# Performance work log

Measured on AMD Instinct MI355X. Metric: run time of the kernel, lower is better.

Reference implementation:

```python
import jax, jax.numpy as jnp
import numpy as np

V = 1024      # token vocab
C = 8         # n_codebooks
T = 256       # seg_len
BP = 4        # block_pairs (n_latent_blocks)
K = 512       # latent_vocab_size (codebook entries)
E = 128       # emb_dim
D = 128       # latent_dim / d_model
BETA = 0.05
NB = 6 * BP   # decoder sequence length = 24
NH = 4
HD = D // NH
FF = 512
R = 8
IN_FLAT = NB * D
OUT = T * C * V
B = 32


def setup_inputs() -> dict:
    key = jax.random.key(0)
    ks = jax.random.split(key, 20)
    n = lambda i, shape, s=0.02: jax.random.normal(ks[i], shape, jnp.float32) * s
    return {
        "tokens_prev": jax.random.randint(ks[0], (B, T, C), 0, V, jnp.int32),
        "tokens_curr": jax.random.randint(ks[1], (B, T, C), 0, V, jnp.int32),
        "tokens_next": jax.random.randint(ks[2], (B, T, C), 0, V, jnp.int32),
        "emb": n(3, (V, E)),
        "conv1_w": n(4, (4 * D, E * C, 3)),
        "conv1_b": jnp.zeros((4 * D,), jnp.float32),
        "conv2_w": n(5, (2 * D, 4 * D, 1)),
        "conv2_b": jnp.zeros((2 * D,), jnp.float32),
        "cb_instru": jax.random.uniform(ks[6], (K, D), jnp.float32, -1.0 / K, 1.0 / K),
        "cb_vocal": jax.random.uniform(ks[7], (K, D), jnp.float32, -1.0 / K, 1.0 / K),
        "pos": n(8, (1, NB, D), 1.0),
        "attn_in_w": n(9, (3 * D, D)),
        "attn_in_b": jnp.zeros((3 * D,), jnp.float32),
        "attn_out_w": n(10, (D, D)),
        "attn_out_b": jnp.zeros((D,), jnp.float32),
        "ln1_g": jnp.ones((D,), jnp.float32),
        "ln1_b": jnp.zeros((D,), jnp.float32),
        "lin1_w": n(11, (FF, D)),
        "lin1_b": jnp.zeros((FF,), jnp.float32),
        "lin2_w": n(12, (D, FF)),
        "lin2_b": jnp.zeros((D,), jnp.float32),
        "ln2_g": jnp.ones((D,), jnp.float32),
        "ln2_b": jnp.zeros((D,), jnp.float32),
        "lora_a": n(13, (R, IN_FLAT), 0.01),
        "lora_b": n(14, (OUT, R), 0.01),
    }


def _conv1d(x, w, b, pad):
    # x: (B, Cin, L), w: (Cout, Cin, Kw)
    y = jax.lax.conv_general_dilated(x, w, window_strides=(1,), padding=[(pad, pad)],
                                     dimension_numbers=("NCH", "OIH", "NCH"))
    return y + b[None, :, None]


def _encode(tokens, emb, w1, b1, w2, b2):
    Bb, Tt, Cc = tokens.shape
    x = emb[tokens].reshape(Bb, Tt, -1).transpose(0, 2, 1)       # (B, C*E, T)
    x = jax.nn.relu(_conv1d(x, w1, b1, 1))                        # (B, 4D, T)
    x = jax.nn.relu(_conv1d(x, w2, b2, 0))                        # (B, 2D, T)
    # AdaptiveAvgPool1d(BP) with T % BP == 0 -> mean over contiguous chunks
    x = x.reshape(Bb, 2 * D, BP, Tt // BP).mean(-1).transpose(0, 2, 1)  # (B, BP, 2D)
    return x[..., :D], x[..., D:]


def _vq(z, codebook):
    # z: (B, N, D); eval-mode VQ (no EMA update)
    Bb, N, Dd = z.shape
    flat = z.reshape(-1, Dd)
    dist = (jnp.sum(flat * flat, axis=1, keepdims=True)
            - 2.0 * flat @ codebook.T
            + jnp.sum(codebook * codebook, axis=1))
    codes = jnp.argmin(dist, axis=1)
    z_q = codebook[codes].reshape(Bb, N, Dd)
    commit = jnp.mean((z - jax.lax.stop_gradient(z_q)) ** 2)
    loss = BETA * commit
    z_q_st = z + jax.lax.stop_gradient(z_q - z)
    return z_q_st, codes.reshape(Bb, N), loss


def _layer_norm(x, g, b):
    mu = x.mean(-1, keepdims=True)
    var = ((x - mu) ** 2).mean(-1, keepdims=True)
    return (x - mu) * jax.lax.rsqrt(var + 1e-5) * g + b


def _tf_layer(x, in_w, in_b, out_w, out_b, g1, b1, w1, bb1, w2, bb2, g2, b2):
    # Post-norm TransformerEncoderLayer (relu, eval/no-dropout). x: (B, S, D)
    Bb, S, Dd = x.shape
    qkv = x @ in_w.T + in_b
    q, k, v = jnp.split(qkv, 3, axis=-1)
    q = q.reshape(Bb, S, NH, HD).transpose(0, 2, 1, 3)
    k = k.reshape(Bb, S, NH, HD).transpose(0, 2, 1, 3)
    v = v.reshape(Bb, S, NH, HD).transpose(0, 2, 1, 3)
    attn = jax.nn.softmax(jnp.einsum("bhsd,bhtd->bhst", q, k) / np.sqrt(HD), axis=-1)
    o = jnp.einsum("bhst,bhtd->bhsd", attn, v).transpose(0, 2, 1, 3).reshape(Bb, S, Dd)
    x = _layer_norm(x + o @ out_w.T + out_b, g1, b1)
    ff = jax.nn.relu(x @ w1.T + bb1) @ w2.T + bb2
    return _layer_norm(x + ff, g2, b2)


def reference(tokens_prev, tokens_curr, tokens_next, emb, conv1_w, conv1_b,
              conv2_w, conv2_b, cb_instru, cb_vocal, pos, attn_in_w, attn_in_b,
              attn_out_w, attn_out_b, ln1_g, ln1_b, lin1_w, lin1_b, lin2_w,
              lin2_b, ln2_g, ln2_b, lora_a, lora_b):
    p_i, p_v = _encode(tokens_prev, emb, conv1_w, conv1_b, conv2_w, conv2_b)
    c_i, c_v = _encode(tokens_curr, emb, conv1_w, conv1_b, conv2_w, conv2_b)
    n_i, n_v = _encode(tokens_next, emb, conv1_w, conv1_b, conv2_w, conv2_b)
    p_i_q, _, l1 = _vq(p_i, cb_instru)
    c_i_q, _, l2 = _vq(c_i, cb_instru)
    n_i_q, _, l3 = _vq(n_i, cb_instru)
    p_v_q, _, l4 = _vq(p_v, cb_vocal)
    c_v_q, _, l5 = _vq(c_v, cb_vocal)
    n_v_q, _, l6 = _vq(n_v, cb_vocal)
    vq_loss = l1 + l2 + l3 + l4 + l5 + l6
    z = jnp.concatenate([p_i_q, p_v_q, c_i_q, c_v_q, n_i_q, n_v_q], axis=1)  # (B, 24, D)
    z = z + pos[:, :z.shape[1], :]
    z = _tf_layer(z, attn_in_w, attn_in_b, attn_out_w, attn_out_b,
                  ln1_g, ln1_b, lin1_w, lin1_b, lin2_w, lin2_b, ln2_g, ln2_b)
    Bb = z.shape[0]
    flat = z.reshape(Bb, -1)
    logits = (flat @ lora_a.T) @ lora_b.T          # (B, T*C*V)
    logits = logits.reshape(Bb, T, C, V)
    logp = jax.nn.log_softmax(logits, axis=-1)
    nll = -jnp.take_along_axis(logp, tokens_curr[..., None].astype(jnp.int32), axis=-1)
    recon_loss = nll.mean()
    total_loss = recon_loss + vq_loss
    return total_loss
```

## Files before the change

### kernel.cpp

```cpp
#include <hip/hip_runtime.h>
#include <hip/hip_bf16.h>
#include <cstdint>
#include <cstddef>

typedef __attribute__((ext_vector_type(8))) short short8;
typedef __attribute__((ext_vector_type(4))) float floatx4;


__device__ __forceinline__ ushort f2bf(float f) {
    union { float f; unsigned int u; } x; x.f = f;
    unsigned int r = (x.u + 0x7fffu + ((x.u >> 16) & 1u)) >> 16;
    return (ushort)r;
}
__device__ __forceinline__ float bf2f(ushort u) {
    union { unsigned int u; float f; } x; x.u = ((unsigned int)u) << 16;
    return x.f;
}

__global__ __launch_bounds__(256) void prep_all(
    const float* __restrict__ emb, const float* __restrict__ w1,
    const float* __restrict__ w2, const float* __restrict__ cbi,
    const float* __restrict__ cbv, const float* __restrict__ aiw,
    const float* __restrict__ aow, const float* __restrict__ l1w,
    const float* __restrict__ l2w,
    ushort* __restrict__ ebf, ushort* __restrict__ w1bf, ushort* __restrict__ w2bf,
    float* __restrict__ cbiT, float* __restrict__ cbvT,
    ushort* __restrict__ aiwbf, ushort* __restrict__ aowbf,
    ushort* __restrict__ l1wbf, ushort* __restrict__ l2wbf,
    float* __restrict__ accum)
{
    int idx = blockIdx.x * 256 + threadIdx.x;
    if (idx < 4) accum[idx] = 0.f;
    if (idx < 131072) {
        ebf[idx] = f2bf(emb[idx]);
    } else if (idx < 262144) {
        int j = idx - 131072; w2bf[j] = f2bf(w2[j]);
    } else if (idx < 327680) {
        int j = idx - 262144; cbiT[(j & 127) * 512 + (j >> 7)] = cbi[j];
    } else if (idx < 393216) {
        int j = idx - 327680; cbvT[(j & 127) * 512 + (j >> 7)] = cbv[j];
    } else if (idx < 442368) {
        int j = idx - 393216; aiwbf[j] = f2bf(aiw[j]);
    } else if (idx < 475136) {
        int j = idx - 442368; aowbf[j] = f2bf(aow[j]);
    } else if (idx < 540672) {
        int j = idx - 475136; l1wbf[j] = f2bf(l1w[j]);
    } else if (idx < 606208) {
        int j = idx - 540672; l2wbf[j] = f2bf(l2w[j]);
    } else if (idx < 2179072) {
        int j = idx - 606208;
        int e  = j & 127;
        int co = (j >> 7) & 511;
        int cc = (j >> 16) & 7;
        int kw = j >> 19;
        w1bf[j] = f2bf(w1[(co * 1024 + cc * 128 + e) * 3 + kw]);
    }
}

__global__ __launch_bounds__(512, 4) void conv1_mfma(
    const int* __restrict__ tp, const int* __restrict__ tcu, const int* __restrict__ tn,
    const ushort* __restrict__ ebf, const ushort* __restrict__ w1bf,
    const float* __restrict__ b1, ushort* __restrict__ y1)
{
    constexpr int LDA = 136;
    __shared__ ushort As[130 * LDA];
    __shared__ ushort Bs[128 * LDA];
    __shared__ int tokL[130 * 8];
    const int tid = threadIdx.x;
    const int bx = blockIdx.x;
    const int nb = bx & 3, mb = bx >> 2;
    const int set = mb >> 6, rem = mb & 63, bb = rem >> 1, t0 = (rem & 1) << 7;
    const int n0 = nb << 7;
    const int* tok = (set == 0) ? tp : ((set == 1) ? tcu : tn);

    for (int idx = tid; idx < 1040; idx += 512) {
        const int row = idx >> 3, cc = idx & 7;
        const int gt = t0 + row - 1;
        tokL[idx] = (gt >= 0 && gt < 256) ? tok[bb * 2048 + gt * 8 + cc] : -1;
    }

    const int w = tid >> 6, lane = tid & 63;
    const int wm = w & 1, wn = w >> 1;
    const int rA = lane & 15, q4 = lane >> 4;
    const int ch = tid & 15, rowst = tid >> 4;

    floatx4 acc[4][2];
    for (int mi = 0; mi < 4; ++mi)
        for (int ni = 0; ni < 2; ++ni)
            acc[mi][ni] = (floatx4)(0.0f);

    __syncthreads();

    for (int cc = 0; cc < 8; ++cc) {
        for (int p = 0; p < 5; ++p) {
            const int row = p * 32 + rowst;
            if (row < 130) {
                const int tk = tokL[row * 8 + cc];
                uint4 val = make_uint4(0u, 0u, 0u, 0u);
                if (tk >= 0) val = *(const uint4*)(ebf + tk * 128 + ch * 8);
                *(uint4*)(As + row * LDA + ch * 8) = val;
            }
        }
        for (int kw = 0; kw < 3; ++kw) {
            const ushort* wsrc = w1bf + ((size_t)((kw * 8 + cc) * 512 + n0)) * 128;
            for (int p = 0; p < 4; ++p) {
                const int row = p * 32 + rowst;
                *(uint4*)(Bs + row * LDA + ch * 8) = *(const uint4*)(wsrc + row * 128 + ch * 8);
            }
            __syncthreads();
            for (int ks = 0; ks < 4; ++ks) {
                const int k0 = ks * 32 + q4 * 8;
                short8 a[4], bfr[2];
                for (int mi = 0; mi < 4; ++mi)
                    a[mi] = *(const short8*)(As + (wm * 64 + mi * 16 + rA + kw) * LDA + k0);
                for (int ni = 0; ni < 2; ++ni)
                    bfr[ni] = *(const short8*)(Bs + (wn * 32 + ni * 16 + rA) * LDA + k0);
                for (int mi = 0; mi < 4; ++mi)
                    for (int ni = 0; ni < 2; ++ni)
                        acc[mi][ni] = __builtin_amdgcn_mfma_f32_16x16x32_bf16(
                            a[mi], bfr[ni], acc[mi][ni], 0, 0, 0);
            }
            __syncthreads();
        }
    }
    for (int ni = 0; ni < 2; ++ni) {
        const int co = n0 + wn * 32 + ni * 16 + rA;
        const float bias = b1[co];
        for (int mi = 0; mi < 4; ++mi) {
            for (int r = 0; r < 4; ++r) {
                const int t = t0 + wm * 64 + mi * 16 + q4 * 4 + r;
                float v = acc[mi][ni][r] + bias;
                v = v > 0.f ? v : 0.f;
                y1[((size_t)(set * 32 + bb) * 256 + t) * 512 + co] = f2bf(v);
            }
        }
    }
}

__global__ __launch_bounds__(512, 4) void conv2_mfma(
    const ushort* __restrict__ y1, const ushort* __restrict__ w2bf,
    const float* __restrict__ b2, float* __restrict__ y2)
{
    constexpr int LDA = 136;
    __shared__ ushort As[128 * LDA];
    __shared__ ushort Bs[128 * LDA];
    __shared__ float pool[256];
    const int tid = threadIdx.x;
    const int bx = blockIdx.x;
    const int nb = bx & 1, mb = bx >> 1;
    const int set = mb >> 6, rem = mb & 63, bb = rem >> 1, t0 = (rem & 1) << 7;
    const int n0 = nb << 7;
    const int w = tid >> 6, lane = tid & 63;
    const int wm = w & 1, wn = w >> 1;
    const int rA = lane & 15, q4 = lane >> 4;
    const int ch = tid & 15, rowst = tid >> 4;

    floatx4 acc[4][2];
    for (int mi = 0; mi < 4; ++mi)
        for (int ni = 0; ni < 2; ++ni)
            acc[mi][ni] = (floatx4)(0.0f);

    const size_t arowbase = ((size_t)(set * 32 + bb) * 256 + t0) * 512;
    for (int kc = 0; kc < 4; ++kc) {
        for (int p = 0; p < 4; ++p) {
            const int row = p * 32 + rowst;
            *(uint4*)(As + row * LDA + ch * 8) =
                *(const uint4*)(y1 + arowbase + (size_t)row * 512 + kc * 128 + ch * 8);
            *(uint4*)(Bs + row * LDA + ch * 8) =
                *(const uint4*)(w2bf + (size_t)(n0 + row) * 512 + kc * 128 + ch * 8);
        }
        __syncthreads();
        for (int ks = 0; ks < 4; ++ks) {
            const int k0 = ks * 32 + q4 * 8;
            short8 a[4], bfr[2];
            for (int mi = 0; mi < 4; ++mi)
                a[mi] = *(const short8*)(As + (wm * 64 + mi * 16 + rA) * LDA + k0);
            for (int ni = 0; ni < 2; ++ni)
                bfr[ni] = *(const short8*)(Bs + (wn * 32 + ni * 16 + rA) * LDA + k0);
            for (int mi = 0; mi < 4; ++mi)
                for (int ni = 0; ni < 2; ++ni)
                    acc[mi][ni] = __builtin_amdgcn_mfma_f32_16x16x32_bf16(
                        a[mi], bfr[ni], acc[mi][ni], 0, 0, 0);
        }
        __syncthreads();
    }
    for (int ni = 0; ni < 2; ++ni) {
        const int col = wn * 32 + ni * 16 + rA;
        const float bias = b2[n0 + col];
        float s = 0.f;
        for (int mi = 0; mi < 4; ++mi)
            for (int r = 0; r < 4; ++r) {
                float v = acc[mi][ni][r] + bias;
                s += v > 0.f ? v : 0.f;
            }
        s += __shfl_xor(s, 16);
        s += __shfl_xor(s, 32);
        if (q4 == 0) pool[wm * 128 + col] = s;
    }
    __syncthreads();
    if (tid < 256) {
        const int wrow = tid >> 7, col = tid & 127;
        const int p = (t0 >> 6) + wrow;
        y2[((size_t)(set * 32 + bb) * 4 + p) * 256 + n0 + col] = pool[tid] * (1.f / 64.f);
    }
}

__global__ __launch_bounds__(256) void vq_kernel(
    const float* __restrict__ y2, const float* __restrict__ cbiT, const float* __restrict__ cbvT,
    const float* __restrict__ cbi, const float* __restrict__ cbv,
    const float* __restrict__ pos, float* __restrict__ ztr, ushort* __restrict__ xbf,
    float* __restrict__ accum)
{
    const int q = blockIdx.x;
    const int tid = threadIdx.x;
    const int set = q >> 7, bb = (q >> 2) & 31, p = q & 3;
    __shared__ float zloc[256];
    __shared__ float bestv[4];
    __shared__ int   besti[4];
    __shared__ int   code_sh[2];
    __shared__ float wsum2[4];
    zloc[tid] = y2[(size_t)q * 256 + tid];
    __syncthreads();
    const int w = tid >> 6, lane = tid & 63;
    const int half = w >> 1, sub = w & 1;
    const float4* cbT4 = (const float4*)(half ? cbvT : cbiT);
    const float* zh = zloc + half * 128;
    const int k4 = sub * 64 + lane;
    float a0 = 0.f, a1 = 0.f, a2 = 0.f, a3 = 0.f;
    for (int d = 0; d < 128; ++d) {
        float4 v = cbT4[d * 128 + k4];
        const float z = zh[d];
        float d0 = z - v.x, d1 = z - v.y, d2 = z - v.z, d3 = z - v.w;
        a0 += d0 * d0; a1 += d1 * d1; a2 += d2 * d2; a3 += d3 * d3;
    }
    float best = a0; int bidx = k4 * 4;
    if (a1 < best) { best = a1; bidx = k4 * 4 + 1; }
    if (a2 < best) { best = a2; bidx = k4 * 4 + 2; }
    if (a3 < best) { best = a3; bidx = k4 * 4 + 3; }
    for (int off = 32; off > 0; off >>= 1) {
        float ov = __shfl_xor(best, off);
        int   oi = __shfl_xor(bidx, off);
        if (ov < best || (ov == best && oi < bidx)) { best = ov; bidx = oi; }
    }
    if (lane == 0) { bestv[w] = best; besti[w] = bidx; }
    __syncthreads();
    if (tid < 2) {
        float v0 = bestv[tid * 2], v1 = bestv[tid * 2 + 1];
        int   i0 = besti[tid * 2], i1 = besti[tid * 2 + 1];
        code_sh[tid] = (v1 < v0 || (v1 == v0 && i1 < i0)) ? i1 : i0;
    }
    __syncthreads();
    const int hh = tid >> 7, d = tid & 127;
    const int code = code_sh[hh];
    const float* cb = hh ? cbv : cbi;
    const float zq = cb[code * 128 + d];
    const float diff = zloc[hh * 128 + d] - zq;
    float sq = diff * diff;
    for (int off = 32; off > 0; off >>= 1) sq += __shfl_xor(sq, off);
    if (lane == 0) wsum2[w] = sq;
    const int s = (set * 2 + hh) * 4 + p;
    const float val = zq + pos[s * 128 + d];
    ztr[((size_t)bb * 24 + s) * 128 + d] = val;
    xbf[((size_t)bb * 24 + s) * 128 + d] = f2bf(val);
    __syncthreads();
    if (tid == 0) atomicAdd(&accum[0], wsum2[0] + wsum2[1] + wsum2[2] + wsum2[3]);
}

template<int KTOT, int NTOT, int RELU, int OUTBF>
__global__ __launch_bounds__(256) void gemm64_kernel(
    const ushort* __restrict__ A, const ushort* __restrict__ Bw,
    const float* __restrict__ bias, void* __restrict__ Co)
{
    constexpr int NBLK = NTOT / 64;
    constexpr int LDA = 136;
    __shared__ ushort As[64 * LDA];
    __shared__ ushort Bs[64 * LDA];
    const int tid = threadIdx.x;
    const int mblk = blockIdx.x / NBLK, nblk = blockIdx.x % NBLK;
    const int m0 = mblk * 64, n0 = nblk * 64;
    const int w = tid >> 6, lane = tid & 63;
    const int rA = lane & 15, q4 = lane >> 4;
    const int ch = tid & 15, rowst = tid >> 4;

    floatx4 acc[4];
    for (int mi = 0; mi < 4; ++mi) acc[mi] = (floatx4)(0.f);

    for (int kc = 0; kc < KTOT / 128; ++kc) {
        for (int i = 0; i < 4; ++i) {
            const int row = i * 16 + rowst;
            *(uint4*)(As + row * LDA + ch * 8) =
                *(const uint4*)(A + (size_t)(m0 + row) * KTOT + kc * 128 + ch * 8);
            *(uint4*)(Bs + row * LDA + ch * 8) =
                *(const uint4*)(Bw + (size_t)(n0 + row) * KTOT + kc * 128 + ch * 8);
        }
        __syncthreads();
        for (int ks = 0; ks < 4; ++ks) {
            const int k0 = ks * 32 + q4 * 8;
            short8 bfr = *(const short8*)(Bs + (w * 16 + rA) * LDA + k0);
            for (int mi = 0; mi < 4; ++mi) {
                short8 a = *(const short8*)(As + (mi * 16 + rA) * LDA + k0);
                acc[mi] = __builtin_amdgcn_mfma_f32_16x16x32_bf16(a, bfr, acc[mi], 0, 0, 0);
            }
        }
        __syncthreads();
    }
    const int col = n0 + w * 16 + rA;
    const float bs = bias[col];
    for (int mi = 0; mi < 4; ++mi) {
        for (int r = 0; r < 4; ++r) {
            const int row = m0 + mi * 16 + q4 * 4 + r;
            float vv = acc[mi][r] + bs;
            if (RELU) vv = vv > 0.f ? vv : 0.f;
            if (OUTBF) ((ushort*)Co)[(size_t)row * NTOT + col] = f2bf(vv);
            else       ((float*)Co)[(size_t)row * NTOT + col]  = vv;
        }
    }
}

template<int KTOT, int WRITE_F32>
__global__ __launch_bounds__(256) void gemm_ln_kernel(
    const ushort* __restrict__ A, const ushort* __restrict__ Bw,
    const float* __restrict__ bias, const float* __restrict__ resid,
    const float* __restrict__ g, const float* __restrict__ beta,
    ushort* __restrict__ outbf, float* __restrict__ outf)
{
    constexpr int LDA = 136;
    __shared__ ushort As[64 * LDA];
    __shared__ ushort Bs[128 * LDA];
    __shared__ float ps[64 * 4], pq[64 * 4], muv[64], invv[64];
    const int tid = threadIdx.x;
    const int m0 = blockIdx.x * 64;
    const int w = tid >> 6, lane = tid & 63;
    const int rA = lane & 15, q4 = lane >> 4;
    const int ch = tid & 15, rowst = tid >> 4;

    floatx4 acc[4][2];
    for (int mi = 0; mi < 4; ++mi)
        for (int ni = 0; ni < 2; ++ni)
            acc[mi][ni] = (floatx4)(0.f);

    for (int kc = 0; kc < KTOT / 128; ++kc) {
        for (int i = 0; i < 4; ++i) {
            const int row = i * 16 + rowst;
            *(uint4*)(As + row * LDA + ch * 8) =
                *(const uint4*)(A + (size_t)(m0 + row) * KTOT + kc * 128 + ch * 8);
        }
        for (int i = 0; i < 8; ++i) {
            const int row = i * 16 + rowst;
            *(uint4*)(Bs + row * LDA + ch * 8) =
                *(const uint4*)(Bw + (size_t)row * KTOT + kc * 128 + ch * 8);
        }
        __syncthreads();
        for (int ks = 0; ks < 4; ++ks) {
            const int k0 = ks * 32 + q4 * 8;
            short8 a[4], bfr[2];
            for (int mi = 0; mi < 4; ++mi)
                a[mi] = *(const short8*)(As + (mi * 16 + rA) * LDA + k0);
            for (int ni = 0; ni < 2; ++ni)
                bfr[ni] = *(const short8*)(Bs + ((w * 2 + ni) * 16 + rA) * LDA + k0);
            for (int mi = 0; mi < 4; ++mi)
                for (int ni = 0; ni < 2; ++ni)
                    acc[mi][ni] = __builtin_amdgcn_mfma_f32_16x16x32_bf16(
                        a[mi], bfr[ni], acc[mi][ni], 0, 0, 0);
        }
        __syncthreads();
    }
    for (int ni = 0; ni < 2; ++ni) {
        const int col = (w * 2 + ni) * 16 + rA;
        const float bs = bias[col];
        for (int mi = 0; mi < 4; ++mi)
            for (int r = 0; r < 4; ++r) {
                const int row = m0 + mi * 16 + q4 * 4 + r;
                acc[mi][ni][r] += bs + resid[(size_t)row * 128 + col];
            }
    }
    for (int mi = 0; mi < 4; ++mi)
        for (int r = 0; r < 4; ++r) {
            float s  = acc[mi][0][r] + acc[mi][1][r];
            float sq = acc[mi][0][r] * acc[mi][0][r] + acc[mi][1][r] * acc[mi][1][r];
            for (int off = 1; off < 16; off <<= 1) {
                s  += __shfl_xor(s, off);
                sq += __shfl_xor(sq, off);
            }
            if (rA == 0) {
                const int rl = mi * 16 + q4 * 4 + r;
                ps[rl * 4 + w] = s;
                pq[rl * 4 + w] = sq;
            }
        }
    __syncthreads();
    if (tid < 64) {
        float s  = ps[tid * 4] + ps[tid * 4 + 1] + ps[tid * 4 + 2] + ps[tid * 4 + 3];
        float sq = pq[tid * 4] + pq[tid * 4 + 1] + pq[tid * 4 + 2] + pq[tid * 4 + 3];
        float mu = s * (1.f / 128.f);
        float var = sq * (1.f / 128.f) - mu * mu;
        muv[tid] = mu;
        invv[tid] = rsqrtf(var + 1e-5f);
    }
    __syncthreads();
    for (int ni = 0; ni < 2; ++ni) {
        const int col = (w * 2 + ni) * 16 + rA;
        const float gg = g[col], bb = beta[col];
        for (int mi = 0; mi < 4; ++mi)
            for (int r = 0; r < 4; ++r) {
                const int rl = mi * 16 + q4 * 4 + r;
                const int row = m0 + rl;
                float v = (acc[mi][ni][r] - muv[rl]) * invv[rl] * gg + bb;
                outbf[(size_t)row * 128 + col] = f2bf(v);
                if (WRITE_F32) outf[(size_t)row * 128 + col] = v;
            }
    }
}

__global__ __launch_bounds__(64) void attn_kernel(
    const float* __restrict__ qkvb, ushort* __restrict__ obuf)
{
    const int bh = blockIdx.x;
    const int b = bh >> 2, h = bh & 3;
    const int tid = threadIdx.x;
    __shared__ float q[24 * 32], k[24 * 32], v[24 * 32], sc[24 * 24];
    for (int i = 0; i < 12; ++i) {
        const int idx = i * 64 + tid;
        const int s = idx >> 5, d = idx & 31;
        const size_t base = ((size_t)(b * 24 + s)) * 384 + h * 32 + d;
        q[idx] = qkvb[base];
        k[idx] = qkvb[base + 128];
        v[idx] = qkvb[base + 256];
    }
    __syncthreads();
    for (int i = 0; i < 9; ++i) {
        const int e = i * 64 + tid;
        const int si = e / 24, j = e - si * 24;
        float a = 0.f;
        for (int d = 0; d < 32; ++d) a += q[si * 32 + d] * k[j * 32 + d];
        sc[si * 24 + j] = a * 0.17677669529663687f;
    }
    __syncthreads();
    if (tid < 24) {
        float* row = sc + tid * 24;
        float m = row[0];
        for (int j = 1; j < 24; ++j) m = row[j] > m ? row[j] : m;
        float ssum = 0.f;
        for (int j = 0; j < 24; ++j) { float e = __expf(row[j] - m); row[j] = e; ssum += e; }
        float inv = 1.f / ssum;
        for (int j = 0; j < 24; ++j) row[j] *= inv;
    }
    __syncthreads();
    for (int i = 0; i < 12; ++i) {
        const int idx = i * 64 + tid;
        const int s = idx >> 5, d = idx & 31;
        float a = 0.f;
        for (int j = 0; j < 24; ++j) a += sc[s * 24 + j] * v[j * 32 + d];
        obuf[((size_t)(b * 24 + s)) * 128 + h * 32 + d] = f2bf(a);
    }
}

__global__ __launch_bounds__(256) void lora_kernel(
    const ushort* __restrict__ zbf, const float* __restrict__ lora_a,
    float* __restrict__ hbuf)
{
    const int b = blockIdx.x;
    const int tid = threadIdx.x;
    const int w = tid >> 6, lane = tid & 63;
    __shared__ float zl[3072];
    for (int idx = tid; idx < 3072; idx += 256) zl[idx] = bf2f(zbf[(size_t)b * 3072 + idx]);
    __syncthreads();
    for (int rr = 0; rr < 2; ++rr) {
        const int r = w + rr * 4;
        float acc = 0.f;
        for (int idx = lane; idx < 3072; idx += 64)
            acc += lora_a[(size_t)r * 3072 + idx] * zl[idx];
        for (int off = 32; off > 0; off >>= 1) acc += __shfl_xor(acc, off);
        if (lane == 0) hbuf[b * 8 + r] = acc;
    }
}

__global__ __launch_bounds__(256) void logits_kernel(
    const float* __restrict__ hbuf, const float* __restrict__ lora_b,
    const int* __restrict__ tokc, float* __restrict__ accum, float* __restrict__ out)
{
    const int tid = threadIdx.x;
    const int tcb = blockIdx.x;
    __shared__ float hl[256];
    __shared__ float wsum[4];
    __shared__ float ltok;
    hl[tid] = hbuf[tid];
    float wr[4][8];
    for (int i = 0; i < 4; ++i) {
        const float4* pw = (const float4*)(lora_b + ((size_t)tcb * 1024 + tid + 256 * i) * 8);
        float4 x = pw[0], y = pw[1];
        wr[i][0] = x.x; wr[i][1] = x.y; wr[i][2] = x.z; wr[i][3] = x.w;
        wr[i][4] = y.x; wr[i][5] = y.y; wr[i][6] = y.z; wr[i][7] = y.w;
    }
    __syncthreads();
    float nll = 0.f;
    for (int bb = 0; bb < 32; ++bb) {
        const int tv = tokc[bb * 2048 + tcb];
        const float* h = hl + bb * 8;
        float h0 = h[0], h1 = h[1], h2 = h[2], h3 = h[3];
        float h4 = h[4], h5 = h[5], h6 = h[6], h7 = h[7];
        float sl = 0.f;
        for (int i = 0; i < 4; ++i) {
            float lg = h0 * wr[i][0] + h1 * wr[i][1] + h2 * wr[i][2] + h3 * wr[i][3]
                     + h4 * wr[i][4] + h5 * wr[i][5] + h6 * wr[i][6] + h7 * wr[i][7];
            sl += __expf(lg);
            if (tid + 256 * i == tv) ltok = lg;
        }
        for (int off = 32; off > 0; off >>= 1) sl += __shfl_xor(sl, off);
        if ((tid & 63) == 0) wsum[tid >> 6] = sl;
        __syncthreads();
        if (tid == 0) nll += logf(wsum[0] + wsum[1] + wsum[2] + wsum[3]) - ltok;
        __syncthreads();
    }
    if (tid == 0) {
        atomicAdd(&accum[1], nll);
        __threadfence();
        unsigned int prev = atomicAdd((unsigned int*)(accum + 2), 1u);
        if (prev == 2047u) {
            float vq  = atomicAdd(&accum[0], 0.f);
            float rec = atomicAdd(&accum[1], 0.f);
            out[0] = rec * (1.f / 65536.f) + 0.05f * vq * (1.f / 16384.f);
        }
    }
}

extern "C" void kernel_launch(void* const* d_in, const int* in_sizes, int n_in,
                              void* d_out, int out_size, void* d_ws, size_t ws_size,
                              hipStream_t stream) {
    const int*   tp   = (const int*)d_in[0];
    const int*   tcu  = (const int*)d_in[1];
    const int*   tn   = (const int*)d_in[2];
    const float* emb  = (const float*)d_in[3];
    const float* w1   = (const float*)d_in[4];
    const float* b1   = (const float*)d_in[5];
    const float* w2   = (const float*)d_in[6];
    const float* b2   = (const float*)d_in[7];
    const float* cbi  = (const float*)d_in[8];
    const float* cbv  = (const float*)d_in[9];
    const float* pos  = (const float*)d_in[10];
    const float* aiw  = (const float*)d_in[11];
    const float* aib  = (const float*)d_in[12];
    const float* aow  = (const float*)d_in[13];
    const float* aob  = (const float*)d_in[14];
    const float* g1   = (const float*)d_in[15];
    const float* be1  = (const float*)d_in[16];
    const float* l1w  = (const float*)d_in[17];
    const float* l1b  = (const float*)d_in[18];
    const float* l2w  = (const float*)d_in[19];
    const float* l2b  = (const float*)d_in[20];
    const float* g2   = (const float*)d_in[21];
    const float* be2  = (const float*)d_in[22];
    const float* lra  = (const float*)d_in[23];
    const float* lrb  = (const float*)d_in[24];

    char* wsb = (char*)d_ws;
    ushort* ebf  = (ushort*)(wsb + 0);
    ushort* w1bf = (ushort*)(wsb + 262144);
    ushort* w2bf = (ushort*)(wsb + 3407872);
    float*  cbiT = (float*)(wsb + 3670016);
    float*  cbvT = (float*)(wsb + 3932160);
    ushort* y1   = (ushort*)(wsb + 4194304);
    float*  y2   = (float*)(wsb + 29360128);
    float*  ztr  = (float*)(wsb + 29753344);
    float*  hbuf = (float*)(wsb + 30146560);
    float*  accum= (float*)(wsb + 30147584);
    ushort* aiwbf= (ushort*)(wsb + 30147648);
    ushort* aowbf= (ushort*)(wsb + 30245952);
    ushort* l1wbf= (ushort*)(wsb + 30278720);
    ushort* l2wbf= (ushort*)(wsb + 30409792);
    if (ws_size < 30540864) return;

    float*  qkvb = (float*)(wsb + 4194304);
    ushort* obuf = (ushort*)(wsb + 5373952);
    ushort* x1bf = (ushort*)(wsb + 5570560);
    float*  x1f  = (float*)(wsb + 5767168);
    ushort* hff  = (ushort*)(wsb + 6160384);
    ushort* zbf  = (ushort*)(wsb + 6946816);
    ushort* xbf  = (ushort*)(wsb + 7143424);

    prep_all<<<8512, 256, 0, stream>>>(emb, w1, w2, cbi, cbv, aiw, aow, l1w, l2w,
                                       ebf, w1bf, w2bf, cbiT, cbvT,
                                       aiwbf, aowbf, l1wbf, l2wbf, accum);
    conv1_mfma<<<768, 512, 0, stream>>>(tp, tcu, tn, ebf, w1bf, b1, y1);
    conv2_mfma<<<384, 512, 0, stream>>>(y1, w2bf, b2, y2);
    vq_kernel<<<384, 256, 0, stream>>>(y2, cbiT, cbvT, cbi, cbv, pos, ztr, xbf, accum);
    gemm64_kernel<128, 384, 0, 0><<<72, 256, 0, stream>>>(xbf, aiwbf, aib, qkvb);
    attn_kernel<<<128, 64, 0, stream>>>(qkvb, obuf);
    gemm_ln_kernel<128, 1><<<12, 256, 0, stream>>>(obuf, aowbf, aob, ztr, g1, be1, x1bf, x1f);
    gemm64_kernel<128, 512, 1, 1><<<96, 256, 0, stream>>>(x1bf, l1wbf, l1b, hff);
    gemm_ln_kernel<512, 0><<<12, 256, 0, stream>>>(hff, l2wbf, l2b, x1f, g2, be2, zbf, nullptr);
    lora_kernel<<<32, 256, 0, stream>>>(zbf, lra, hbuf);
    logits_kernel<<<2048, 256, 0, stream>>>(hbuf, lrb, tcu, accum, (float*)d_out);
}
```

Measured before the change: 404.4 us.

## Fuse transformer layer and LoRA-A projection into one per-batch tail kernel

Replaces the six small launches (QKV gemm, attention, out-proj+LN, FFN1, FFN2+LN, LoRA-A) with a single kernel, one block per batch element. Each block keeps its 24x128 activations in LDS and streams each weight matrix into LDS in turn. This removes launch overhead and the global round trips for intermediate buffers. In exchange it runs only 32 blocks with about 160KB of LDS each, and every block reloads all weights, which leaves most of the GPU idle for this stage.

```diff
diff --git a/kernel.cpp b/kernel.cpp
--- a/kernel.cpp
+++ b/kernel.cpp
@@ -208,8 +208,7 @@
 __global__ __launch_bounds__(256) void vq_kernel(
     const float* __restrict__ y2, const float* __restrict__ cbiT, const float* __restrict__ cbvT,
     const float* __restrict__ cbi, const float* __restrict__ cbv,
-    const float* __restrict__ pos, float* __restrict__ ztr, ushort* __restrict__ xbf,
-    float* __restrict__ accum)
+    const float* __restrict__ pos, float* __restrict__ ztr, float* __restrict__ accum)
 {
     const int q = blockIdx.x;
     const int tid = threadIdx.x;
@@ -259,219 +258,277 @@
     for (int off = 32; off > 0; off >>= 1) sq += __shfl_xor(sq, off);
     if (lane == 0) wsum2[w] = sq;
     const int s = (set * 2 + hh) * 4 + p;
-    const float val = zq + pos[s * 128 + d];
-    ztr[((size_t)bb * 24 + s) * 128 + d] = val;
-    xbf[((size_t)bb * 24 + s) * 128 + d] = f2bf(val);
+    ztr[((size_t)bb * 24 + s) * 128 + d] = zq + pos[s * 128 + d];
     __syncthreads();
     if (tid == 0) atomicAdd(&accum[0], wsum2[0] + wsum2[1] + wsum2[2] + wsum2[3]);
 }
 
-template<int KTOT, int NTOT, int RELU, int OUTBF>
-__global__ __launch_bounds__(256) void gemm64_kernel(
-    const ushort* __restrict__ A, const ushort* __restrict__ Bw,
-    const float* __restrict__ bias, void* __restrict__ Co)
+__global__ __launch_bounds__(256) void tail_kernel(
+    const float* __restrict__ ztr,
+    const ushort* __restrict__ aiwbf, const float* __restrict__ aib,
+    const ushort* __restrict__ aowbf, const float* __restrict__ aob,
+    const float* __restrict__ g1, const float* __restrict__ be1,
+    const ushort* __restrict__ l1wbf, const float* __restrict__ l1b,
+    const ushort* __restrict__ l2wbf, const float* __restrict__ l2b,
+    const float* __restrict__ g2, const float* __restrict__ be2,
+    const float* __restrict__ lora_a, float* __restrict__ hbuf)
 {
-    constexpr int NBLK = NTOT / 64;
-    constexpr int LDA = 136;
-    __shared__ ushort As[64 * LDA];
-    __shared__ ushort Bs[64 * LDA];
-    const int tid = threadIdx.x;
-    const int mblk = blockIdx.x / NBLK, nblk = blockIdx.x % NBLK;
-    const int m0 = mblk * 64, n0 = nblk * 64;
-    const int w = tid >> 6, lane = tid & 63;
-    const int rA = lane & 15, q4 = lane >> 4;
-    const int ch = tid & 15, rowst = tid >> 4;
-
-    floatx4 acc[4];
-    for (int mi = 0; mi < 4; ++mi) acc[mi] = (floatx4)(0.f);
-
-    for (int kc = 0; kc < KTOT / 128; ++kc) {
-        for (int i = 0; i < 4; ++i) {
-            const int row = i * 16 + rowst;
-            *(uint4*)(As + row * LDA + ch * 8) =
-                *(const uint4*)(A + (size_t)(m0 + row) * KTOT + kc * 128 + ch * 8);
-            *(uint4*)(Bs + row * LDA + ch * 8) =
-                *(const uint4*)(Bw + (size_t)(n0 + row) * KTOT + kc * 128 + ch * 8);
-        }
-        __syncthreads();
-        for (int ks = 0; ks < 4; ++ks) {
-            const int k0 = ks * 32 + q4 * 8;
-            short8 bfr = *(const short8*)(Bs + (w * 16 + rA) * LDA + k0);
-            for (int mi = 0; mi < 4; ++mi) {
-                short8 a = *(const short8*)(As + (mi * 16 + rA) * LDA + k0);
-                acc[mi] = __builtin_amdgcn_mfma_f32_16x16x32_bf16(a, bfr, acc[mi], 0, 0, 0);
-            }
-        }
-        __syncthreads();
-    }
-    const int col = n0 + w * 16 + rA;
-    const float bs = bias[col];
-    for (int mi = 0; mi < 4; ++mi) {
-        for (int r = 0; r < 4; ++r) {
-            const int row = m0 + mi * 16 + q4 * 4 + r;
-            float vv = acc[mi][r] + bs;
-            if (RELU) vv = vv > 0.f ? vv : 0.f;
-            if (OUTBF) ((ushort*)Co)[(size_t)row * NTOT + col] = f2bf(vv);
-            else       ((float*)Co)[(size_t)row * NTOT + col]  = vv;
-        }
-    }
-}
-
-template<int KTOT, int WRITE_F32>
-__global__ __launch_bounds__(256) void gemm_ln_kernel(
-    const ushort* __restrict__ A, const ushort* __restrict__ Bw,
-    const float* __restrict__ bias, const float* __restrict__ resid,
-    const float* __restrict__ g, const float* __restrict__ beta,
-    ushort* __restrict__ outbf, float* __restrict__ outf)
-{
-    constexpr int LDA = 136;
-    __shared__ ushort As[64 * LDA];
-    __shared__ ushort Bs[128 * LDA];
-    __shared__ float ps[64 * 4], pq[64 * 4], muv[64], invv[64];
-    const int tid = threadIdx.x;
-    const int m0 = blockIdx.x * 64;
-    const int w = tid >> 6, lane = tid & 63;
-    const int rA = lane & 15, q4 = lane >> 4;
-    const int ch = tid & 15, rowst = tid >> 4;
-
-    floatx4 acc[4][2];
-    for (int mi = 0; mi < 4; ++mi)
-        for (int ni = 0; ni < 2; ++ni)
-            acc[mi][ni] = (floatx4)(0.f);
-
-    for (int kc = 0; kc < KTOT / 128; ++kc) {
-        for (int i = 0; i < 4; ++i) {
-            const int row = i * 16 + rowst;
-            *(uint4*)(As + row * LDA + ch * 8) =
-                *(const uint4*)(A + (size_t)(m0 + row) * KTOT + kc * 128 + ch * 8);
-        }
-        for (int i = 0; i < 8; ++i) {
-            const int row = i * 16 + rowst;
-            *(uint4*)(Bs + row * LDA + ch * 8) =
-                *(const uint4*)(Bw + (size_t)row * KTOT + kc * 128 + ch * 8);
-        }
-        __syncthreads();
-        for (int ks = 0; ks < 4; ++ks) {
-            const int k0 = ks * 32 + q4 * 8;
-            short8 a[4], bfr[2];
-            for (int mi = 0; mi < 4; ++mi)
-                a[mi] = *(const short8*)(As + (mi * 16 + rA) * LDA + k0);
-            for (int ni = 0; ni < 2; ++ni)
-                bfr[ni] = *(const short8*)(Bs + ((w * 2 + ni) * 16 + rA) * LDA + k0);
-            for (int mi = 0; mi < 4; ++mi)
-                for (int ni = 0; ni < 2; ++ni)
-                    acc[mi][ni] = __builtin_amdgcn_mfma_f32_16x16x32_bf16(
-                        a[mi], bfr[ni], acc[mi][ni], 0, 0, 0);
-        }
-        __syncthreads();
-    }
-    for (int ni = 0; ni < 2; ++ni) {
-        const int col = (w * 2 + ni) * 16 + rA;
-        const float bs = bias[col];
-        for (int mi = 0; mi < 4; ++mi)
-            for (int r = 0; r < 4; ++r) {
-                const int row = m0 + mi * 16 + q4 * 4 + r;
-                acc[mi][ni][r] += bs + resid[(size_t)row * 128 + col];
-            }
-    }
-    for (int mi = 0; mi < 4; ++mi)
-        for (int r = 0; r < 4; ++r) {
-            float s  = acc[mi][0][r] + acc[mi][1][r];
-            float sq = acc[mi][0][r] * acc[mi][0][r] + acc[mi][1][r] * acc[mi][1][r];
-            for (int off = 1; off < 16; off <<= 1) {
-                s  += __shfl_xor(s, off);
-                sq += __shfl_xor(sq, off);
-            }
-            if (rA == 0) {
-                const int rl = mi * 16 + q4 * 4 + r;
-                ps[rl * 4 + w] = s;
-                pq[rl * 4 + w] = sq;
-            }
-        }
-    __syncthreads();
-    if (tid < 64) {
-        float s  = ps[tid * 4] + ps[tid * 4 + 1] + ps[tid * 4 + 2] + ps[tid * 4 + 3];
-        float sq = pq[tid * 4] + pq[tid * 4 + 1] + pq[tid * 4 + 2] + pq[tid * 4 + 3];
-        float mu = s * (1.f / 128.f);
-        float var = sq * (1.f / 128.f) - mu * mu;
-        muv[tid] = mu;
-        invv[tid] = rsqrtf(var + 1e-5f);
-    }
-    __syncthreads();
-    for (int ni = 0; ni < 2; ++ni) {
-        const int col = (w * 2 + ni) * 16 + rA;
-        const float gg = g[col], bb = beta[col];
-        for (int mi = 0; mi < 4; ++mi)
-            for (int r = 0; r < 4; ++r) {
-                const int rl = mi * 16 + q4 * 4 + r;
-                const int row = m0 + rl;
-                float v = (acc[mi][ni][r] - muv[rl]) * invv[rl] * gg + bb;
-                outbf[(size_t)row * 128 + col] = f2bf(v);
-                if (WRITE_F32) outf[(size_t)row * 128 + col] = v;
-            }
-    }
-}
-
-__global__ __launch_bounds__(64) void attn_kernel(
-    const float* __restrict__ qkvb, ushort* __restrict__ obuf)
-{
-    const int bh = blockIdx.x;
-    const int b = bh >> 2, h = bh & 3;
-    const int tid = threadIdx.x;
-    __shared__ float q[24 * 32], k[24 * 32], v[24 * 32], sc[24 * 24];
-    for (int i = 0; i < 12; ++i) {
-        const int idx = i * 64 + tid;
-        const int s = idx >> 5, d = idx & 31;
-        const size_t base = ((size_t)(b * 24 + s)) * 384 + h * 32 + d;
-        q[idx] = qkvb[base];
-        k[idx] = qkvb[base + 128];
-        v[idx] = qkvb[base + 256];
-    }
-    __syncthreads();
-    for (int i = 0; i < 9; ++i) {
-        const int e = i * 64 + tid;
-        const int si = e / 24, j = e - si * 24;
-        float a = 0.f;
-        for (int d = 0; d < 32; ++d) a += q[si * 32 + d] * k[j * 32 + d];
-        sc[si * 24 + j] = a * 0.17677669529663687f;
-    }
-    __syncthreads();
-    if (tid < 24) {
-        float* row = sc + tid * 24;
-        float m = row[0];
-        for (int j = 1; j < 24; ++j) m = row[j] > m ? row[j] : m;
-        float ssum = 0.f;
-        for (int j = 0; j < 24; ++j) { float e = __expf(row[j] - m); row[j] = e; ssum += e; }
-        float inv = 1.f / ssum;
-        for (int j = 0; j < 24; ++j) row[j] *= inv;
-    }
-    __syncthreads();
-    for (int i = 0; i < 12; ++i) {
-        const int idx = i * 64 + tid;
-        const int s = idx >> 5, d = idx & 31;
-        float a = 0.f;
-        for (int j = 0; j < 24; ++j) a += sc[s * 24 + j] * v[j * 32 + d];
-        obuf[((size_t)(b * 24 + s)) * 128 + h * 32 + d] = f2bf(a);
-    }
-}
-
-__global__ __launch_bounds__(256) void lora_kernel(
-    const ushort* __restrict__ zbf, const float* __restrict__ lora_a,
-    float* __restrict__ hbuf)
-{
+    __shared__ __align__(16) char LDSC[162304];
+    float*  Xf  = (float*)LDSC;
+    ushort* Abf = (ushort*)(LDSC + 12288);
+    char*   S   = LDSC + 20992;
+    ushort* Wq  = (ushort*)S;
+    float*  QKV = (float*)(S + 104448);
+    float*  Ssc = (float*)S;
+    ushort* Wo  = (ushort*)S;
+    ushort* W1  = (ushort*)S;
+    ushort* Hbf = (ushort*)S;
+    ushort* Wh  = (ushort*)(S + 34304);
+    float*  ps  = (float*)(S + 104448);
+    float*  pq  = (float*)(S + 104960);
+    float*  muv = (float*)(S + 105472);
+    float*  inv = (float*)(S + 105600);
+
     const int b = blockIdx.x;
     const int tid = threadIdx.x;
     const int w = tid >> 6, lane = tid & 63;
-    __shared__ float zl[3072];
-    for (int idx = tid; idx < 3072; idx += 256) zl[idx] = bf2f(zbf[(size_t)b * 3072 + idx]);
-    __syncthreads();
+    const int rA = lane & 15, q4 = lane >> 4;
+
+    for (int i = tid; i < 544; i += 256) ((uint4*)Abf)[i] = make_uint4(0u, 0u, 0u, 0u);
+    __syncthreads();
+    for (int i = tid; i < 3072; i += 256) {
+        float v = ztr[(size_t)b * 3072 + i];
+        Xf[i] = v;
+        Abf[(i >> 7) * 136 + (i & 127)] = f2bf(v);
+    }
+    for (int i = tid; i < 6144; i += 256) {
+        const int row = i >> 4, ch = i & 15;
+        *(uint4*)(Wq + row * 136 + ch * 8) = *(const uint4*)(aiwbf + row * 128 + ch * 8);
+    }
+    __syncthreads();
+
+    {
+        floatx4 acc[2][6];
+        for (int mi = 0; mi < 2; ++mi) for (int ni = 0; ni < 6; ++ni) acc[mi][ni] = (floatx4)(0.f);
+        for (int ks = 0; ks < 4; ++ks) {
+            const int k0 = ks * 32 + q4 * 8;
+            short8 a[2];
+            for (int mi = 0; mi < 2; ++mi)
+                a[mi] = *(const short8*)(Abf + (mi * 16 + rA) * 136 + k0);
+            for (int ni = 0; ni < 6; ++ni) {
+                short8 bfr = *(const short8*)(Wq + ((w * 6 + ni) * 16 + rA) * 136 + k0);
+                for (int mi = 0; mi < 2; ++mi)
+                    acc[mi][ni] = __builtin_amdgcn_mfma_f32_16x16x32_bf16(a[mi], bfr, acc[mi][ni], 0, 0, 0);
+            }
+        }
+        for (int ni = 0; ni < 6; ++ni) {
+            const int col = (w * 6 + ni) * 16 + rA;
+            const float bs = aib[col];
+            for (int mi = 0; mi < 2; ++mi)
+                for (int r = 0; r < 4; ++r) {
+                    const int row = mi * 16 + q4 * 4 + r;
+                    if (row < 24) QKV[row * 384 + col] = acc[mi][ni][r] + bs;
+                }
+        }
+    }
+    __syncthreads();
+
+    {
+        const int h = w;
+        for (int l = 0; l < 9; ++l) {
+            const int e = l * 64 + lane;
+            const int i = e / 24, j = e - i * 24;
+            float s = 0.f;
+            for (int d = 0; d < 32; ++d)
+                s += QKV[i * 384 + h * 32 + d] * QKV[j * 384 + 128 + h * 32 + d];
+            Ssc[w * 576 + i * 24 + j] = s * 0.17677669529663687f;
+        }
+        __syncthreads();
+        if (lane < 24) {
+            float* row = Ssc + w * 576 + lane * 24;
+            float m = row[0];
+            for (int j = 1; j < 24; ++j) m = row[j] > m ? row[j] : m;
+            float ssum = 0.f;
+            for (int j = 0; j < 24; ++j) { float e = __expf(row[j] - m); row[j] = e; ssum += e; }
+            float iv = 1.f / ssum;
+            for (int j = 0; j < 24; ++j) row[j] *= iv;
+        }
+        __syncthreads();
+        for (int l = 0; l < 12; ++l) {
+            const int idx = l * 64 + lane;
+            const int s = idx >> 5, d = idx & 31;
+            float a = 0.f;
+            for (int j = 0; j < 24; ++j)
+                a += Ssc[w * 576 + s * 24 + j] * QKV[j * 384 + 256 + h * 32 + d];
+            Abf[s * 136 + h * 32 + d] = f2bf(a);
+        }
+    }
+    __syncthreads();
+
+    for (int i = tid; i < 2048; i += 256) {
+        const int row = i >> 4, ch = i & 15;
+        *(uint4*)(Wo + row * 136 + ch * 8) = *(const uint4*)(aowbf + row * 128 + ch * 8);
+    }
+    __syncthreads();
+    {
+        floatx4 acc[2][2];
+        for (int mi = 0; mi < 2; ++mi) for (int ni = 0; ni < 2; ++ni) acc[mi][ni] = (floatx4)(0.f);
+        for (int ks = 0; ks < 4; ++ks) {
+            const int k0 = ks * 32 + q4 * 8;
+            short8 a[2];
+            for (int mi = 0; mi < 2; ++mi)
+                a[mi] = *(const short8*)(Abf + (mi * 16 + rA) * 136 + k0);
+            for (int ni = 0; ni < 2; ++ni) {
+                short8 bfr = *(const short8*)(Wo + ((w * 2 + ni) * 16 + rA) * 136 + k0);
+                for (int mi = 0; mi < 2; ++mi)
+                    acc[mi][ni] = __builtin_amdgcn_mfma_f32_16x16x32_bf16(a[mi], bfr, acc[mi][ni], 0, 0, 0);
+            }
+        }
+        for (int ni = 0; ni < 2; ++ni) {
+            const int col = (w * 2 + ni) * 16 + rA;
+            const float bs = aob[col];
+            for (int mi = 0; mi < 2; ++mi)
+                for (int r = 0; r < 4; ++r) {
+                    const int row = mi * 16 + q4 * 4 + r;
+                    acc[mi][ni][r] += bs + (row < 24 ? Xf[row * 128 + col] : 0.f);
+                }
+        }
+        for (int mi = 0; mi < 2; ++mi)
+            for (int r = 0; r < 4; ++r) {
+                float s  = acc[mi][0][r] + acc[mi][1][r];
+                float sq = acc[mi][0][r] * acc[mi][0][r] + acc[mi][1][r] * acc[mi][1][r];
+                for (int off = 1; off < 16; off <<= 1) { s += __shfl_xor(s, off); sq += __shfl_xor(sq, off); }
+                if (rA == 0) { const int rl = mi * 16 + q4 * 4 + r; ps[rl * 4 + w] = s; pq[rl * 4 + w] = sq; }
+            }
+        __syncthreads();
+        if (tid < 32) {
+            float s  = ps[tid * 4] + ps[tid * 4 + 1] + ps[tid * 4 + 2] + ps[tid * 4 + 3];
+            float sq = pq[tid * 4] + pq[tid * 4 + 1] + pq[tid * 4 + 2] + pq[tid * 4 + 3];
+            float mu = s * (1.f / 128.f);
+            float var = sq * (1.f / 128.f) - mu * mu;
+            muv[tid] = mu; inv[tid] = rsqrtf(var + 1e-5f);
+        }
+        __syncthreads();
+        for (int ni = 0; ni < 2; ++ni) {
+            const int col = (w * 2 + ni) * 16 + rA;
+            const float gg = g1[col], bb2 = be1[col];
+            for (int mi = 0; mi < 2; ++mi)
+                for (int r = 0; r < 4; ++r) {
+                    const int rl = mi * 16 + q4 * 4 + r;
+                    if (rl < 24) {
+                        float v = (acc[mi][ni][r] - muv[rl]) * inv[rl] * gg + bb2;
+                        Xf[rl * 128 + col] = v;
+                        Abf[rl * 136 + col] = f2bf(v);
+                    }
+                }
+        }
+    }
+    __syncthreads();
+
+    for (int i = tid; i < 8192; i += 256) {
+        const int row = i >> 4, ch = i & 15;
+        *(uint4*)(W1 + row * 136 + ch * 8) = *(const uint4*)(l1wbf + row * 128 + ch * 8);
+    }
+    __syncthreads();
+    {
+        floatx4 acc[2][8];
+        for (int mi = 0; mi < 2; ++mi) for (int ni = 0; ni < 8; ++ni) acc[mi][ni] = (floatx4)(0.f);
+        for (int ks = 0; ks < 4; ++ks) {
+            const int k0 = ks * 32 + q4 * 8;
+            short8 a[2];
+            for (int mi = 0; mi < 2; ++mi)
+                a[mi] = *(const short8*)(Abf + (mi * 16 + rA) * 136 + k0);
+            for (int ni = 0; ni < 8; ++ni) {
+                short8 bfr = *(const short8*)(W1 + ((w * 8 + ni) * 16 + rA) * 136 + k0);
+                for (int mi = 0; mi < 2; ++mi)
+                    acc[mi][ni] = __builtin_amdgcn_mfma_f32_16x16x32_bf16(a[mi], bfr, acc[mi][ni], 0, 0, 0);
+            }
+        }
+        __syncthreads();
+        for (int i = tid; i < 536; i += 256) ((uint4*)(Hbf + 24 * 536))[i] = make_uint4(0u, 0u, 0u, 0u);
+        for (int ni = 0; ni < 8; ++ni) {
+            const int col = (w * 8 + ni) * 16 + rA;
+            const float bs = l1b[col];
+            for (int mi = 0; mi < 2; ++mi)
+                for (int r = 0; r < 4; ++r) {
+                    const int row = mi * 16 + q4 * 4 + r;
+                    if (row < 24) {
+                        float v = acc[mi][ni][r] + bs;
+                        Hbf[row * 536 + col] = f2bf(v > 0.f ? v : 0.f);
+                    }
+                }
+        }
+    }
+    __syncthreads();
+
+    {
+        floatx4 acc[2][2];
+        for (int mi = 0; mi < 2; ++mi) for (int ni = 0; ni < 2; ++ni) acc[mi][ni] = (floatx4)(0.f);
+        for (int kh = 0; kh < 2; ++kh) {
+            for (int i = tid; i < 4096; i += 256) {
+                const int row = i >> 5, ch = i & 31;
+                *(uint4*)(Wh + row * 264 + ch * 8) =
+                    *(const uint4*)(l2wbf + row * 512 + kh * 256 + ch * 8);
+            }
+            __syncthreads();
+            for (int ks = 0; ks < 8; ++ks) {
+                const int k0 = ks * 32 + q4 * 8;
+                short8 a[2];
+                for (int mi = 0; mi < 2; ++mi)
+                    a[mi] = *(const short8*)(Hbf + (mi * 16 + rA) * 536 + kh * 256 + k0);
+                for (int ni = 0; ni < 2; ++ni) {
+                    short8 bfr = *(const short8*)(Wh + ((w * 2 + ni) * 16 + rA) * 264 + k0);
+                    for (int mi = 0; mi < 2; ++mi)
+                        acc[mi][ni] = __builtin_amdgcn_mfma_f32_16x16x32_bf16(a[mi], bfr, acc[mi][ni], 0, 0, 0);
+                }
+            }
+            __syncthreads();
+        }
+        for (int ni = 0; ni < 2; ++ni) {
+            const int col = (w * 2 + ni) * 16 + rA;
+            const float bs = l2b[col];
+            for (int mi = 0; mi < 2; ++mi)
+                for (int r = 0; r < 4; ++r) {
+                    const int row = mi * 16 + q4 * 4 + r;
+                    acc[mi][ni][r] += bs + (row < 24 ? Xf[row * 128 + col] : 0.f);
+                }
+        }
+        for (int mi = 0; mi < 2; ++mi)
+            for (int r = 0; r < 4; ++r) {
+                float s  = acc[mi][0][r] + acc[mi][1][r];
+                float sq = acc[mi][0][r] * acc[mi][0][r] + acc[mi][1][r] * acc[mi][1][r];
+                for (int off = 1; off < 16; off <<= 1) { s += __shfl_xor(s, off); sq += __shfl_xor(sq, off); }
+                if (rA == 0) { const int rl = mi * 16 + q4 * 4 + r; ps[rl * 4 + w] = s; pq[rl * 4 + w] = sq; }
+            }
+        __syncthreads();
+        if (tid < 32) {
+            float s  = ps[tid * 4] + ps[tid * 4 + 1] + ps[tid * 4 + 2] + ps[tid * 4 + 3];
+            float sq = pq[tid * 4] + pq[tid * 4 + 1] + pq[tid * 4 + 2] + pq[tid * 4 + 3];
+            float mu = s * (1.f / 128.f);
+            float var = sq * (1.f / 128.f) - mu * mu;
+            muv[tid] = mu; inv[tid] = rsqrtf(var + 1e-5f);
+        }
+        __syncthreads();
+        for (int ni = 0; ni < 2; ++ni) {
+            const int col = (w * 2 + ni) * 16 + rA;
+            const float gg = g2[col], bb2 = be2[col];
+            for (int mi = 0; mi < 2; ++mi)
+                for (int r = 0; r < 4; ++r) {
+                    const int rl = mi * 16 + q4 * 4 + r;
+                    if (rl < 24)
+                        Xf[rl * 128 + col] = (acc[mi][ni][r] - muv[rl]) * inv[rl] * gg + bb2;
+                }
+        }
+    }
+    __syncthreads();
+
     for (int rr = 0; rr < 2; ++rr) {
         const int r = w + rr * 4;
-        float acc = 0.f;
-        for (int idx = lane; idx < 3072; idx += 64)
-            acc += lora_a[(size_t)r * 3072 + idx] * zl[idx];
-        for (int off = 32; off > 0; off >>= 1) acc += __shfl_xor(acc, off);
-        if (lane == 0) hbuf[b * 8 + r] = acc;
+        float a = 0.f;
+        for (int i = lane; i < 3072; i += 64)
+            a += lora_a[(size_t)r * 3072 + i] * Xf[i];
+        for (int off = 32; off > 0; off >>= 1) a += __shfl_xor(a, off);
+        if (lane == 0) hbuf[b * 8 + r] = a;
     }
 }
 
@@ -570,25 +627,13 @@
     ushort* l2wbf= (ushort*)(wsb + 30409792);
     if (ws_size < 30540864) return;
 
-    float*  qkvb = (float*)(wsb + 4194304);
-    ushort* obuf = (ushort*)(wsb + 5373952);
-    ushort* x1bf = (ushort*)(wsb + 5570560);
-    float*  x1f  = (float*)(wsb + 5767168);
-    ushort* hff  = (ushort*)(wsb + 6160384);
-    ushort* zbf  = (ushort*)(wsb + 6946816);
-    ushort* xbf  = (ushort*)(wsb + 7143424);
-
     prep_all<<<8512, 256, 0, stream>>>(emb, w1, w2, cbi, cbv, aiw, aow, l1w, l2w,
                                        ebf, w1bf, w2bf, cbiT, cbvT,
                                        aiwbf, aowbf, l1wbf, l2wbf, accum);
     conv1_mfma<<<768, 512, 0, stream>>>(tp, tcu, tn, ebf, w1bf, b1, y1);
     conv2_mfma<<<384, 512, 0, stream>>>(y1, w2bf, b2, y2);
-    vq_kernel<<<384, 256, 0, stream>>>(y2, cbiT, cbvT, cbi, cbv, pos, ztr, xbf, accum);
-    gemm64_kernel<128, 384, 0, 0><<<72, 256, 0, stream>>>(xbf, aiwbf, aib, qkvb);
-    attn_kernel<<<128, 64, 0, stream>>>(qkvb, obuf);
-    gemm_ln_kernel<128, 1><<<12, 256, 0, stream>>>(obuf, aowbf, aob, ztr, g1, be1, x1bf, x1f);
-    gemm64_kernel<128, 512, 1, 1><<<96, 256, 0, stream>>>(x1bf, l1wbf, l1b, hff);
-    gemm_ln_kernel<512, 0><<<12, 256, 0, stream>>>(hff, l2wbf, l2b, x1f, g2, be2, zbf, nullptr);
-    lora_kernel<<<32, 256, 0, stream>>>(zbf, lra, hbuf);
+    vq_kernel<<<384, 256, 0, stream>>>(y2, cbiT, cbvT, cbi, cbv, pos, ztr, accum);
+    tail_kernel<<<32, 256, 0, stream>>>(ztr, aiwbf, aib, aowbf, aob, g1, be1,
+                                        l1wbf, l1b, l2wbf, l2b, g2, be2, lra, hbuf);
     logits_kernel<<<2048, 256, 0, stream>>>(hbuf, lrb, tcu, accum, (float*)d_out);
 }
```

New measurement: 409.8 us. Within noise of the previous version (+1.3%).
